# Performance work log

Hardware: AMD Instinct MI355X
Metric: run time of the kernel (lower is better)

The kernel has to match this reference:

```python
import jax, jax.numpy as jnp
import numpy as np

LAG = 1  # from init_kwargs

def _from_embedding(z, lag):
    # torch loop: out[i] = z[i] for i < lag; out[i] = z[i] + detach(out[i-lag]) otherwise.
    # For i grouped by residue class mod lag this is a cumulative sum along dim 0.
    # The detach means gradients flow only through the direct z[i] term (identity grad),
    # so forward = cumsum, and we restore detach semantics with stop_gradient.
    N = z.shape[0]
    assert N % lag == 0, "sequence length must be a multiple of lag"
    zg = z.reshape(N // lag, lag, *z.shape[1:])        # [G, lag, B, D]
    cum = jnp.cumsum(zg, axis=0).reshape(z.shape)       # [N, B, D]
    # forward value = cum; backward: d(out)/d(z) = identity (accumulated prefix detached)
    return jax.lax.stop_gradient(cum - z) + z

def setup_inputs() -> dict:
    key = jax.random.key(0)
    k1, = jax.random.split(key, 1)
    z = jax.random.normal(k1, (8192, 64, 128), dtype=jnp.float32)
    previous_loss = jnp.zeros((1,), dtype=jnp.float32)
    return {"z": z, "previous_loss": previous_loss}

def reference(z, previous_loss):
    z_delagged = _from_embedding(z, LAG)
    return (z_delagged, previous_loss)
```

## Files before the change

kernel.cpp:

```cpp
#include <hip/hip_runtime.h>


typedef float f4 __attribute__((ext_vector_type(4)));

constexpr int NROWS = 8192;
constexpr int NCOLS = 8192;
constexpr int NCOL4 = NCOLS / 4;
constexpr int TPB   = 256;
constexpr int KCH   = 128;
constexpr int RR    = NROWS / KCH;
constexpr int CT    = NCOL4 / TPB;

__global__ __launch_bounds__(TPB) void k_partial(const f4* __restrict__ z,
                                                 f4* __restrict__ agg,
                                                 const float* __restrict__ prev,
                                                 float* __restrict__ out_tail) {
    const int tile  = blockIdx.x & (CT - 1);
    const int chunk = blockIdx.x >> 3;
    const int c4    = tile * TPB + threadIdx.x;
    if (blockIdx.x == 0 && threadIdx.x == 0) out_tail[0] = prev[0];
    const f4* p = z + (size_t)chunk * RR * NCOL4 + c4;
    f4 a = (f4)0.f;
    #pragma unroll 8
    for (int r = 0; r < RR; ++r) a += p[(size_t)r * NCOL4];
    agg[(size_t)chunk * NCOL4 + c4] = a;
}

__global__ __launch_bounds__(TPB) void k_apply(const f4* __restrict__ z,
                                               const f4* __restrict__ agg,
                                               f4* __restrict__ out) {
    const int tile  = blockIdx.x & (CT - 1);
    const int chunk = KCH - 1 - (blockIdx.x >> 3);
    const int c4    = tile * TPB + threadIdx.x;

    f4 s = (f4)0.f;
    const f4* ap = agg + c4;
    #pragma unroll 8
    for (int cp = 0; cp < chunk; ++cp) s += ap[(size_t)cp * NCOL4];

    const f4* p = z   + (size_t)chunk * RR * NCOL4 + c4;
    f4*       q = out + (size_t)chunk * RR * NCOL4 + c4;
    #pragma unroll 4
    for (int r = 0; r < RR; ++r) {
        s += p[(size_t)r * NCOL4];
        __builtin_nontemporal_store(s, &q[(size_t)r * NCOL4]);
    }
}

extern "C" void kernel_launch(void* const* d_in, const int* in_sizes, int n_in,
                              void* d_out, int out_size, void* d_ws, size_t ws_size,
                              hipStream_t stream) {
    const f4*    z    = (const f4*)d_in[0];
    const float* prev = (const float*)d_in[1];
    float*       out  = (float*)d_out;
    float*       tail = out + (size_t)NROWS * NCOLS;
    f4*          agg  = (f4*)d_ws;

    k_partial<<<KCH * CT, TPB, 0, stream>>>(z, agg, prev, tail);
    k_apply<<<KCH * CT, TPB, 0, stream>>>(z, (const f4*)agg, (f4*)out);
}
```

Before: 139.0 us.

## Compute chunk prefix sums once via last-block scan instead of per-block reduction

The partial kernel now ends with an atomic counter per column tile, and the last block to finish scans the chunk aggregates into exclusive prefixes. The apply kernel then reads a single prefix value instead of summing up to 127 aggregates per block. Nontemporal loads and larger unroll factors are added as well. The cost is an extra memset launch and a serial 128-step scan in the last block of each tile.

```diff
diff --git a/kernel.cpp b/kernel.cpp
--- a/kernel.cpp
+++ b/kernel.cpp
@@ -11,19 +11,46 @@
 constexpr int RR    = NROWS / KCH;
 constexpr int CT    = NCOL4 / TPB;
 
-__global__ __launch_bounds__(TPB) void k_partial(const f4* __restrict__ z,
-                                                 f4* __restrict__ agg,
-                                                 const float* __restrict__ prev,
-                                                 float* __restrict__ out_tail) {
+__global__ __launch_bounds__(TPB) void k_partial_scan(
+    const f4* __restrict__ z, f4* __restrict__ agg,
+    unsigned int* __restrict__ cnt,
+    const float* __restrict__ prev, float* __restrict__ out_tail)
+{
     const int tile  = blockIdx.x & (CT - 1);
     const int chunk = blockIdx.x >> 3;
-    const int c4    = tile * TPB + threadIdx.x;
-    if (blockIdx.x == 0 && threadIdx.x == 0) out_tail[0] = prev[0];
+    const int tid   = threadIdx.x;
+    const int c4    = tile * TPB + tid;
+
+    if (blockIdx.x == 0 && tid == 0) out_tail[0] = prev[0];
+
     const f4* p = z + (size_t)chunk * RR * NCOL4 + c4;
     f4 a = (f4)0.f;
-    #pragma unroll 8
-    for (int r = 0; r < RR; ++r) a += p[(size_t)r * NCOL4];
+    #pragma unroll 16
+    for (int r = 0; r < RR; ++r)
+        a += __builtin_nontemporal_load(&p[(size_t)r * NCOL4]);
     agg[(size_t)chunk * NCOL4 + c4] = a;
+
+    __shared__ int lastFlag;
+    __syncthreads();
+    if (tid == 0) {
+        __threadfence();
+        unsigned int old = __hip_atomic_fetch_add(&cnt[tile], 1u,
+                                                  __ATOMIC_ACQ_REL,
+                                                  __HIP_MEMORY_SCOPE_AGENT);
+        lastFlag = (old == KCH - 1);
+    }
+    __syncthreads();
+    if (!lastFlag) return;
+
+    __builtin_amdgcn_fence(__ATOMIC_ACQUIRE, "agent");
+    f4 run = (f4)0.f;
+    f4* ap = agg + c4;
+    #pragma unroll 16
+    for (int k = 0; k < KCH; ++k) {
+        f4 t = ap[(size_t)k * NCOL4];
+        ap[(size_t)k * NCOL4] = run;
+        run += t;
+    }
 }
 
 __global__ __launch_bounds__(TPB) void k_apply(const f4* __restrict__ z,
@@ -33,16 +60,12 @@
     const int chunk = KCH - 1 - (blockIdx.x >> 3);
     const int c4    = tile * TPB + threadIdx.x;
 
-    f4 s = (f4)0.f;
-    const f4* ap = agg + c4;
-    #pragma unroll 8
-    for (int cp = 0; cp < chunk; ++cp) s += ap[(size_t)cp * NCOL4];
-
+    f4 s = agg[(size_t)chunk * NCOL4 + c4];
     const f4* p = z   + (size_t)chunk * RR * NCOL4 + c4;
     f4*       q = out + (size_t)chunk * RR * NCOL4 + c4;
-    #pragma unroll 4
+    #pragma unroll 8
     for (int r = 0; r < RR; ++r) {
-        s += p[(size_t)r * NCOL4];
+        s += __builtin_nontemporal_load(&p[(size_t)r * NCOL4]);
         __builtin_nontemporal_store(s, &q[(size_t)r * NCOL4]);
     }
 }
@@ -54,8 +77,12 @@
     const float* prev = (const float*)d_in[1];
     float*       out  = (float*)d_out;
     float*       tail = out + (size_t)NROWS * NCOLS;
-    f4*          agg  = (f4*)d_ws;
 
-    k_partial<<<KCH * CT, TPB, 0, stream>>>(z, agg, prev, tail);
+    f4*           agg = (f4*)d_ws;
+    unsigned int* cnt = (unsigned int*)((char*)d_ws +
+                        (size_t)KCH * NCOL4 * sizeof(f4));
+
+    hipMemsetAsync(cnt, 0, CT * sizeof(unsigned int), stream);
+    k_partial_scan<<<KCH * CT, TPB, 0, stream>>>(z, agg, cnt, prev, tail);
     k_apply<<<KCH * CT, TPB, 0, stream>>>(z, (const f4*)agg, (f4*)out);
 }
```

Measured after the change: 268.6 us. 93.2% more time.
